# Kernel tuning notes

Hardware: AMD Instinct MI355X
Metric: run time of the kernel (lower is better)

Reference implementation:

```python
import jax, jax.numpy as jnp
import numpy as np
import math

SQ, SK, B, NP, HN = 2048, 2048, 2, 16, 128
LAYER_NUM = 1  # coeff
NORM_FACTOR = math.sqrt(2048 / 16) * LAYER_NUM  # sqrt(HIDDEN/HEADS) * coeff
SCALE = float(LAYER_NUM)  # MLSASoftmax scale


def setup_inputs() -> dict:
    key = jax.random.key(0)
    kq, kk, kv = jax.random.split(key, 3)
    query_layer = jax.random.normal(kq, (SQ, B, NP, HN), dtype=jnp.float32)
    key_layer = jax.random.normal(kk, (SK, B, NP, HN), dtype=jnp.float32)
    value_layer = jax.random.normal(kv, (SK, B, NP, HN), dtype=jnp.float32)
    # Causal mask: True = masked, shape [b, 1, sq, sk] (broadcasts over heads)
    causal = jnp.triu(jnp.ones((SQ, SK), dtype=bool), k=1)
    attention_mask = jnp.broadcast_to(causal[None, None], (B, 1, SQ, SK))
    return {
        "query_layer": query_layer,
        "key_layer": key_layer,
        "value_layer": value_layer,
        "attention_mask": attention_mask,
    }


def reference(query_layer, key_layer, value_layer, attention_mask):
    # scores[b,n,s,t] = (Q . K) / norm_factor, then * coeff in softmax
    scores = jnp.einsum("sbnh,tbnh->bnst", query_layer, key_layer) / NORM_FACTOR
    scores = scores * SCALE
    scores = jnp.where(attention_mask, jnp.float32(-10000.0), scores)
    # Module computes exp/sum WITHOUT max-subtraction; replicate exactly.
    exp_mo = jnp.exp(scores)
    denomi = jnp.sum(exp_mo, axis=-1, keepdims=True)  # [b, np, sq, 1]
    probs = exp_mo / denomi
    # dropout is identity in eval / for deterministic baseline
    ctx = jnp.einsum("bnst,tbnh->sbnh", probs, value_layer)  # [sq, b, np, hn]
    sq, b, n, h = ctx.shape
    context_layer = ctx.reshape(sq, b, n * h)
    return (context_layer, denomi)
```

## Files before the change

kernel.cpp:

```cpp
#include <hip/hip_runtime.h>
#include <hip/hip_bf16.h>
#include <stdint.h>

typedef __attribute__((ext_vector_type(8))) short short8;
typedef __attribute__((ext_vector_type(8))) unsigned short ushort8;
typedef __attribute__((ext_vector_type(4))) float f32x4;
typedef __attribute__((ext_vector_type(4))) int int4v;

#define NHEAD 32
#define SEQ   2048
#define HN    128

static constexpr float INV_NORM = 0.08838834764831845f;

__device__ __forceinline__ unsigned short f2bf(float f) {
  union { float f; unsigned u; } v; v.f = f;
  unsigned r = v.u + 0x7fffu + ((v.u >> 16) & 1u);
  return (unsigned short)(r >> 16);
}

__device__ __forceinline__ f32x4 mfma16(short8 a, short8 b, f32x4 c) {
  return __builtin_amdgcn_mfma_f32_16x16x32_bf16(a, b, c, 0, 0, 0);
}

__device__ __forceinline__ void gl_lds16(const void* g, void* l) {
  __builtin_amdgcn_global_load_lds(
      (const __attribute__((address_space(1))) unsigned int*)g,
      (__attribute__((address_space(3))) unsigned int*)l, 16, 0, 0);
}

__global__ __launch_bounds__(256) void prep_kv(const float* __restrict__ K,
                                               const float* __restrict__ V,
                                               unsigned short* __restrict__ kswz,
                                               unsigned short* __restrict__ vT) {
  __shared__ unsigned short lds[128 * 136];
  int bid = blockIdx.x;
  int tid = threadIdx.x;
  if (bid < 4096) {
    int idx = bid * 256 + tid;
    int cl = idx & 15;
    int t  = (idx >> 4) & 2047;
    int bn = idx >> 15;
    const float4* src = (const float4*)(K + ((size_t)t * 32 + bn) * 128 + cl * 8);
    float4 a = src[0], b = src[1];
    ushort8 o;
    o[0]=f2bf(a.x); o[1]=f2bf(a.y); o[2]=f2bf(a.z); o[3]=f2bf(a.w);
    o[4]=f2bf(b.x); o[5]=f2bf(b.y); o[6]=f2bf(b.z); o[7]=f2bf(b.w);
    *(ushort8*)(kswz + ((size_t)bn * 2048 + t) * 128 + ((cl ^ (t & 7)) * 8)) = o;
  } else {
    int vb = bid - 4096;
    int bn = vb >> 4;
    int t0 = (vb & 15) << 7;
    int r = tid >> 1, h0 = (tid & 1) * 64;
    const float* src = V + ((size_t)(t0 + r) * 32 + bn) * 128 + h0;
#pragma unroll
    for (int j = 0; j < 8; ++j) {
      float4 a = *(const float4*)(src + j * 8);
      float4 b = *(const float4*)(src + j * 8 + 4);
      ushort8 o;
      o[0]=f2bf(a.x); o[1]=f2bf(a.y); o[2]=f2bf(a.z); o[3]=f2bf(a.w);
      o[4]=f2bf(b.x); o[5]=f2bf(b.y); o[6]=f2bf(b.z); o[7]=f2bf(b.w);
      *(ushort8*)&lds[r * 136 + h0 + j * 8] = o;
    }
    __syncthreads();
    int h = tid >> 1, ts = (tid & 1) * 64;
    unsigned short tmp[64];
#pragma unroll
    for (int j = 0; j < 64; ++j) {
      int p = j & 31;
      int tloc = ((p >> 3) & 3) * 4 + ((p >> 2) & 1) * 16 + (p & 3);
      tmp[j] = lds[(ts + (j & 32) + tloc) * 136 + h];
    }
    ushort8* dst = (ushort8*)(vT + ((size_t)bn * 128 + h) * 2048 + t0 + ts);
#pragma unroll
    for (int j = 0; j < 8; ++j) dst[j] = *(ushort8*)&tmp[j * 8];
  }
}

__device__ __forceinline__ void read_kf(const char* kb, int l15, int hi,
                                        short8 (&kf)[2][4]) {
  int xr = (l15 & 7) << 4;
#pragma unroll
  for (int nt = 0; nt < 2; ++nt) {
    const char* krow = kb + (nt * 16 + l15) * 256;
#pragma unroll
    for (int kk = 0; kk < 4; ++kk)
      kf[nt][kk] = *(const short8*)(krow + (((kk * 4 + hi) * 16) ^ xr));
  }
}

__device__ __forceinline__ void read_vf(const char* vbh, int l15, int hi,
                                        short8 (&vf)[8]) {
#pragma unroll
  for (int ht = 0; ht < 8; ++ht)
    vf[ht] = *(const short8*)(vbh + (ht * 16 + l15) * 64 +
                              ((((l15 >> 1) + hi) & 3) * 16));
}

__device__ __forceinline__ short8 packp(const float (&e)[8], float& da) {
  da += ((e[0] + e[1]) + (e[2] + e[3])) + ((e[4] + e[5]) + (e[6] + e[7]));
  unsigned w0, w1, w2, w3;
  asm("v_cvt_pk_bf16_f32 %0, %1, %2" : "=v"(w0) : "v"(e[0]), "v"(e[1]));
  asm("v_cvt_pk_bf16_f32 %0, %1, %2" : "=v"(w1) : "v"(e[2]), "v"(e[3]));
  asm("v_cvt_pk_bf16_f32 %0, %1, %2" : "=v"(w2) : "v"(e[4]), "v"(e[5]));
  asm("v_cvt_pk_bf16_f32 %0, %1, %2" : "=v"(w3) : "v"(e[6]), "v"(e[7]));
  union { int4v u; short8 s; } pk;
  pk.u = (int4v){(int)w0, (int)w1, (int)w2, (int)w3};
  return pk.s;
}

__device__ __forceinline__ short8 softp_m(const f32x4 (&sv)[2], int t0h, int qbase,
                                          int l15, int hi, float& da) {
  float e[8];
#pragma unroll
  for (int nt = 0; nt < 2; ++nt)
#pragma unroll
    for (int i = 0; i < 4; ++i) {
      float x = __expf(sv[nt][i]);
      int kv = t0h + nt * 16 + hi * 4 + i;
      e[nt * 4 + i] = (kv <= qbase + l15) ? x : 0.0f;
    }
  return packp(e, da);
}

__device__ __forceinline__ short8 softp_u(const f32x4 (&sv)[2], float& da) {
  float e[8];
#pragma unroll
  for (int nt = 0; nt < 2; ++nt)
#pragma unroll
    for (int i = 0; i < 4; ++i)
      e[nt * 4 + i] = __expf(sv[nt][i]);
  return packp(e, da);
}

__global__ __launch_bounds__(512, 2) void attn_main(const float* __restrict__ Q,
                                                    const unsigned short* __restrict__ kswz,
                                                    const unsigned short* __restrict__ vT,
                                                    float* __restrict__ out) {
  __shared__ char smem[65536];
  int tid = threadIdx.x;
  int lane = tid & 63;
  int w = tid >> 6;
  int l15 = lane & 15;
  int hi = lane >> 4;

  int bid = blockIdx.x;
  int bn = bid & 31;
  int z = bid >> 5;
  int qt = (z < 8) ? (15 - z) : (z - 8);
  int qb = qt * 128 + w * 16;
  int ntile = 2 * qt + 2;

  short8 qf[4];
  {
    const float* qrow = Q + ((size_t)(qb + l15) * 32 + bn) * 128;
#pragma unroll
    for (int kk = 0; kk < 4; ++kk) {
      float4 a = *(const float4*)(qrow + kk * 32 + hi * 8);
      float4 b = *(const float4*)(qrow + kk * 32 + hi * 8 + 4);
      short8 o;
      o[0]=(short)f2bf(a.x*INV_NORM); o[1]=(short)f2bf(a.y*INV_NORM);
      o[2]=(short)f2bf(a.z*INV_NORM); o[3]=(short)f2bf(a.w*INV_NORM);
      o[4]=(short)f2bf(b.x*INV_NORM); o[5]=(short)f2bf(b.y*INV_NORM);
      o[6]=(short)f2bf(b.z*INV_NORM); o[7]=(short)f2bf(b.w*INV_NORM);
      qf[kk] = o;
    }
  }

  f32x4 zz = {0.f, 0.f, 0.f, 0.f};
  f32x4 acc[8];
#pragma unroll
  for (int ht = 0; ht < 8; ++ht) acc[ht] = zz;
  float dacc = 0.f;

  const char* kg = (const char*)(kswz + (size_t)bn * 2048 * 128);
  const char* vg = (const char*)(vT + (size_t)bn * 128 * 2048);

  auto stage = [&](int buf, int t0) {
    const char* ksrc = kg + (size_t)t0 * 256;
    char* kl = smem + buf * 16384;
    int c = tid;
#pragma unroll
    for (int rr = 0; rr < 2; ++rr)
      gl_lds16(ksrc + (size_t)(c + rr * 512) * 16, kl + (c + rr * 512) * 16);
    char* vl = smem + 32768 + buf * 16384;
#pragma unroll
    for (int s = 0; s < 2; ++s) {
      int h = c >> 2, sp = c & 3;
      int sl = (sp - (h >> 1)) & 3;
      gl_lds16(vg + (size_t)h * 4096 + (t0 + s * 32) * 2 + sl * 16,
               vl + s * 8192 + c * 16);
    }
  };

  asm volatile("s_waitcnt vmcnt(0)" ::: "memory");
  stage(0, 0);

  int cur = 0;
  for (int it = 0; it < ntile; ++it) {
    int t0 = it * 64;
    asm volatile("s_waitcnt vmcnt(0)" ::: "memory");
    __builtin_amdgcn_s_barrier();
    if (it + 1 < ntile) stage(cur ^ 1, t0 + 64);

    const char* kb = smem + cur * 16384;
    const char* vb = smem + 32768 + cur * 16384;
#pragma unroll
    for (int half = 0; half < 2; ++half) {
      int t0h = t0 + half * 32;
      if (t0h <= qb + 15) {
        const char* kbh = kb + half * 8192;
        const char* vbh = vb + half * 8192;
        short8 kf[2][4];
        read_kf(kbh, l15, hi, kf);
        f32x4 sv[2] = {zz, zz};
        __builtin_amdgcn_s_setprio(1);
#pragma unroll
        for (int nt = 0; nt < 2; ++nt)
#pragma unroll
          for (int kk = 0; kk < 4; ++kk)
            sv[nt] = mfma16(kf[nt][kk], qf[kk], sv[nt]);
        __builtin_amdgcn_s_setprio(0);
        short8 vf[8];
        read_vf(vbh, l15, hi, vf);
        bool mask = (t0h + 31 > qb);
        short8 p = mask ? softp_m(sv, t0h, qb, l15, hi, dacc)
                        : softp_u(sv, dacc);
        __builtin_amdgcn_s_setprio(1);
#pragma unroll
        for (int ht = 0; ht < 8; ++ht)
          acc[ht] = mfma16(p, vf[ht], acc[ht]);
        __builtin_amdgcn_s_setprio(0);
      }
    }
    cur ^= 1;
  }

  {
    float d = dacc;
    d += __shfl_xor(d, 16);
    d += __shfl_xor(d, 32);
    dacc = d;
  }
  float* dn = out + 8388608;
  if (hi == 0) dn[(size_t)bn * 2048 + qb + l15] = dacc;

  float inv[4];
#pragma unroll
  for (int i = 0; i < 4; ++i)
    inv[i] = __builtin_amdgcn_rcpf(__shfl(dacc, hi * 4 + i));

#pragma unroll
  for (int i = 0; i < 4; ++i) {
    float* orow = out + (size_t)(qb + hi * 4 + i) * 4096 + bn * 128 + l15;
#pragma unroll
    for (int ht = 0; ht < 8; ++ht)
      orow[ht * 16] = acc[ht][i] * inv[i];
  }
}

extern "C" void kernel_launch(void* const* d_in, const int* in_sizes, int n_in,
                              void* d_out, int out_size, void* d_ws, size_t ws_size,
                              hipStream_t stream) {
  const float* Q = (const float*)d_in[0];
  const float* K = (const float*)d_in[1];
  const float* V = (const float*)d_in[2];
  float* out = (float*)d_out;

  unsigned short* kswz = (unsigned short*)d_ws;
  unsigned short* vT   = kswz + (size_t)NHEAD * SEQ * HN;

  prep_kv<<<4608, 256, 0, stream>>>(K, V, kswz, vT);
  attn_main<<<512, 512, 0, stream>>>(Q, kswz, vT, out);
}
```

Measured before the change: 80.74 us.

## Pre-pack V into MFMA fragment order and load directly from global memory

The prep kernel now writes V in exact per-lane MFMA B-fragment order, so the attention kernel can read each V fragment with coalesced 16-byte global loads straight into registers. The V staging through LDS and its double buffer are removed, which halves shared memory use and drops the LDS read traffic for V. The cost is that global load latency is now exposed inside the inner loop, with no software pipelining, and every wave in a block re-reads the same V tiles, relying on cache hits.

```diff
diff --git a/kernel.cpp b/kernel.cpp
--- a/kernel.cpp
+++ b/kernel.cpp
@@ -32,7 +32,7 @@
 __global__ __launch_bounds__(256) void prep_kv(const float* __restrict__ K,
                                                const float* __restrict__ V,
                                                unsigned short* __restrict__ kswz,
-                                               unsigned short* __restrict__ vT) {
+                                               unsigned short* __restrict__ vfr) {
   __shared__ unsigned short lds[128 * 136];
   int bid = blockIdx.x;
   int tid = threadIdx.x;
@@ -71,9 +71,15 @@
       int tloc = ((p >> 3) & 3) * 4 + ((p >> 2) & 1) * 16 + (p & 3);
       tmp[j] = lds[(ts + (j & 32) + tloc) * 136 + h];
     }
-    ushort8* dst = (ushort8*)(vT + ((size_t)bn * 128 + h) * 2048 + t0 + ts);
-#pragma unroll
-    for (int j = 0; j < 8; ++j) dst[j] = *(ushort8*)&tmp[j * 8];
+#pragma unroll
+    for (int j = 0; j < 8; ++j) {
+      int c0 = t0 + ts + j * 8;
+      int tg = c0 >> 5;
+      int hv = (c0 >> 3) & 3;
+      size_t du = (size_t)bn * 32768 + (size_t)tg * 512 +
+                  (h >> 4) * 64 + hv * 16 + (h & 15);
+      *(ushort8*)(vfr + du * 8) = *(ushort8*)&tmp[j * 8];
+    }
   }
 }
 
@@ -87,14 +93,6 @@
     for (int kk = 0; kk < 4; ++kk)
       kf[nt][kk] = *(const short8*)(krow + (((kk * 4 + hi) * 16) ^ xr));
   }
-}
-
-__device__ __forceinline__ void read_vf(const char* vbh, int l15, int hi,
-                                        short8 (&vf)[8]) {
-#pragma unroll
-  for (int ht = 0; ht < 8; ++ht)
-    vf[ht] = *(const short8*)(vbh + (ht * 16 + l15) * 64 +
-                              ((((l15 >> 1) + hi) & 3) * 16));
 }
 
 __device__ __forceinline__ short8 packp(const float (&e)[8], float& da) {
@@ -135,9 +133,9 @@
 
 __global__ __launch_bounds__(512, 2) void attn_main(const float* __restrict__ Q,
                                                     const unsigned short* __restrict__ kswz,
-                                                    const unsigned short* __restrict__ vT,
+                                                    const unsigned short* __restrict__ vfr,
                                                     float* __restrict__ out) {
-  __shared__ char smem[65536];
+  __shared__ char smem[32768];
   int tid = threadIdx.x;
   int lane = tid & 63;
   int w = tid >> 6;
@@ -174,23 +172,14 @@
   float dacc = 0.f;
 
   const char* kg = (const char*)(kswz + (size_t)bn * 2048 * 128);
-  const char* vg = (const char*)(vT + (size_t)bn * 128 * 2048);
+  const char* vg = (const char*)vfr + (size_t)bn * 524288;
 
   auto stage = [&](int buf, int t0) {
     const char* ksrc = kg + (size_t)t0 * 256;
     char* kl = smem + buf * 16384;
-    int c = tid;
 #pragma unroll
     for (int rr = 0; rr < 2; ++rr)
-      gl_lds16(ksrc + (size_t)(c + rr * 512) * 16, kl + (c + rr * 512) * 16);
-    char* vl = smem + 32768 + buf * 16384;
-#pragma unroll
-    for (int s = 0; s < 2; ++s) {
-      int h = c >> 2, sp = c & 3;
-      int sl = (sp - (h >> 1)) & 3;
-      gl_lds16(vg + (size_t)h * 4096 + (t0 + s * 32) * 2 + sl * 16,
-               vl + s * 8192 + c * 16);
-    }
+      gl_lds16(ksrc + (size_t)(tid + rr * 512) * 16, kl + (tid + rr * 512) * 16);
   };
 
   asm volatile("s_waitcnt vmcnt(0)" ::: "memory");
@@ -204,15 +193,18 @@
     if (it + 1 < ntile) stage(cur ^ 1, t0 + 64);
 
     const char* kb = smem + cur * 16384;
-    const char* vb = smem + 32768 + cur * 16384;
 #pragma unroll
     for (int half = 0; half < 2; ++half) {
       int t0h = t0 + half * 32;
       if (t0h <= qb + 15) {
         const char* kbh = kb + half * 8192;
-        const char* vbh = vb + half * 8192;
+        const char* vbg = vg + (size_t)(it * 2 + half) * 8192;
         short8 kf[2][4];
         read_kf(kbh, l15, hi, kf);
+        short8 vf[8];
+#pragma unroll
+        for (int ht = 0; ht < 8; ++ht)
+          vf[ht] = *(const short8*)(vbg + ht * 1024 + lane * 16);
         f32x4 sv[2] = {zz, zz};
         __builtin_amdgcn_s_setprio(1);
 #pragma unroll
@@ -221,8 +213,6 @@
           for (int kk = 0; kk < 4; ++kk)
             sv[nt] = mfma16(kf[nt][kk], qf[kk], sv[nt]);
         __builtin_amdgcn_s_setprio(0);
-        short8 vf[8];
-        read_vf(vbh, l15, hi, vf);
         bool mask = (t0h + 31 > qb);
         short8 p = mask ? softp_m(sv, t0h, qb, l15, hi, dacc)
                         : softp_u(sv, dacc);
@@ -268,8 +258,8 @@
   float* out = (float*)d_out;
 
   unsigned short* kswz = (unsigned short*)d_ws;
-  unsigned short* vT   = kswz + (size_t)NHEAD * SEQ * HN;
-
-  prep_kv<<<4608, 256, 0, stream>>>(K, V, kswz, vT);
-  attn_main<<<512, 512, 0, stream>>>(Q, kswz, vT, out);
-}
+  unsigned short* vfr  = kswz + (size_t)NHEAD * SEQ * HN;
+
+  prep_kv<<<4608, 256, 0, stream>>>(K, V, kswz, vfr);
+  attn_main<<<512, 512, 0, stream>>>(Q, kswz, vfr, out);
+}
```

Result: slower. 97.07 us (+20.2%).
